# Kernel optimization log

Measured on AMD Instinct MI355X. Metric: run time of the kernel, lower is better.

## Reference

```python
import jax, jax.numpy as jnp
import numpy as np

N = 50000      # nodes
E = 800000     # edges
D_IN = 128
HID = 32
HEADS = 4
D_OUT = 64
NEG_SLOPE = 0.2  # DGL GATConv default


def gat_layer(feat, W, attn_l, attn_r, bias, src, dst, H, F):
    """One DGL-style GATConv layer. feat:[N,in], W:[in,H*F], attn:[H,F], bias:[H*F]."""
    n = feat.shape[0]
    hp = (feat @ W).reshape(n, H, F)                      # projected features [N,H,F]
    el = jnp.sum(hp * attn_l, axis=-1)                    # [N,H]
    er = jnp.sum(hp * attn_r, axis=-1)                    # [N,H]
    e = jax.nn.leaky_relu(el[src] + er[dst], NEG_SLOPE)   # per-edge score [E,H]
    # segment softmax over incoming edges of each dst node
    m = jax.ops.segment_max(e, dst, num_segments=n)       # [N,H]
    a = jnp.exp(e - m[dst])
    denom = jax.ops.segment_sum(a, dst, num_segments=n)   # [N,H]
    alpha = a / denom[dst]                                # [E,H]
    msg = alpha[:, :, None] * hp[src]                     # [E,H,F]
    out = jax.ops.segment_sum(msg, dst, num_segments=n)   # [N,H,F]
    return out + bias.reshape(1, H, F)


def setup_inputs() -> dict:
    key = jax.random.key(0)
    ks = jax.random.split(key, 12)
    s = 0.05
    x = jax.random.normal(ks[0], (N, D_IN), dtype=jnp.float32)
    src = jax.random.randint(ks[1], (E,), 0, N)
    dst = jax.random.randint(ks[2], (E,), 0, N)
    # layer 1: D_IN -> HID with HEADS heads
    W1 = jax.random.normal(ks[3], (D_IN, HEADS * HID), dtype=jnp.float32) * s
    al1 = jax.random.normal(ks[4], (HEADS, HID), dtype=jnp.float32) * s
    ar1 = jax.random.normal(ks[5], (HEADS, HID), dtype=jnp.float32) * s
    b1 = jnp.zeros((HEADS * HID,), dtype=jnp.float32)
    # layer 2: HID*HEADS -> D_OUT with 1 head
    W2 = jax.random.normal(ks[6], (HID * HEADS, D_OUT), dtype=jnp.float32) * s
    al2 = jax.random.normal(ks[7], (1, D_OUT), dtype=jnp.float32) * s
    ar2 = jax.random.normal(ks[8], (1, D_OUT), dtype=jnp.float32) * s
    b2 = jnp.zeros((D_OUT,), dtype=jnp.float32)
    return {"x": x, "W1": W1, "al1": al1, "ar1": ar1, "b1": b1,
            "W2": W2, "al2": al2, "ar2": ar2, "b2": b2,
            "src": src, "dst": dst}


def reference(x, W1, al1, ar1, b1, W2, al2, ar2, b2, src, dst):
    h1 = gat_layer(x, W1, al1, ar1, b1, src, dst, HEADS, HID)   # [N,HEADS,HID]
    h1 = h1.reshape(N, HEADS * HID)                              # concat heads
    h2 = gat_layer(h1, W2, al2, ar2, b2, src, dst, 1, D_OUT)     # [N,1,D_OUT]
    return h2.reshape(N, D_OUT)                                  # squeeze head dim
```

## Files before the change

kernel.cpp:

```cpp
#include <hip/hip_runtime.h>

#define NEG_SLOPE 0.2f

static __device__ __forceinline__ unsigned short f2bf(float f) {
  unsigned x = __float_as_uint(f);
  return (unsigned short)((x + 0x7FFFu + ((x >> 16) & 1u)) >> 16);
}
static __device__ __forceinline__ float bf2f(unsigned short u) {
  return __uint_as_float((unsigned)u << 16);
}

template<int NCOLS, int H>
__global__ __launch_bounds__(256) void gemm_eler(const float* __restrict__ A,
    const float* __restrict__ B, const float* __restrict__ al, const float* __restrict__ ar,
    unsigned short* __restrict__ hb, float* __restrict__ el, float* __restrict__ er, int M) {
  constexpr int K = 128;
  constexpr int TM = 64;
  constexpr int F = NCOLS / H;
  __shared__ float As[TM][K];
  const int tid = threadIdx.x;
  const int m0 = blockIdx.x * TM;

  for (int i = tid; i < TM * K / 4; i += 256) {
    const int m = (i * 4) / K, k = (i * 4) % K;
    float4 v = make_float4(0.f, 0.f, 0.f, 0.f);
    if (m0 + m < M) v = *reinterpret_cast<const float4*>(&A[(size_t)(m0 + m) * K + k]);
    *reinterpret_cast<float4*>(&As[m][k]) = v;
  }
  __syncthreads();

  constexpr int CW = NCOLS / 32;
  const int c0 = (tid & 31) * CW;
  const int n0 = (tid >> 5) * 8;
  float acc[8][CW];
  #pragma unroll
  for (int i = 0; i < 8; ++i)
    #pragma unroll
    for (int j = 0; j < CW; ++j) acc[i][j] = 0.f;

  #pragma unroll 4
  for (int k = 0; k < K; ++k) {
    float wv[CW];
    if constexpr (CW == 4)
      *reinterpret_cast<float4*>(&wv[0]) = *reinterpret_cast<const float4*>(&B[(size_t)k * NCOLS + c0]);
    else
      *reinterpret_cast<float2*>(&wv[0]) = *reinterpret_cast<const float2*>(&B[(size_t)k * NCOLS + c0]);
    float xv[8];
    #pragma unroll
    for (int i = 0; i < 8; ++i) xv[i] = As[n0 + i][k];
    #pragma unroll
    for (int i = 0; i < 8; ++i)
      #pragma unroll
      for (int j = 0; j < CW; ++j)
        acc[i][j] = fmaf(xv[i], wv[j], acc[i][j]);
  }

  float alv[CW], arv[CW];
  if constexpr (CW == 4) {
    *reinterpret_cast<float4*>(&alv[0]) = *reinterpret_cast<const float4*>(&al[c0]);
    *reinterpret_cast<float4*>(&arv[0]) = *reinterpret_cast<const float4*>(&ar[c0]);
  } else {
    *reinterpret_cast<float2*>(&alv[0]) = *reinterpret_cast<const float2*>(&al[c0]);
    *reinterpret_cast<float2*>(&arv[0]) = *reinterpret_cast<const float2*>(&ar[c0]);
  }
  constexpr int GRP = F / CW;
  const int h = c0 / F;

  #pragma unroll
  for (int i = 0; i < 8; ++i) {
    const int m = m0 + n0 + i;
    if (m < M) {
      if constexpr (CW == 4) {
        ushort4 u;
        u.x = f2bf(acc[i][0]); u.y = f2bf(acc[i][1]);
        u.z = f2bf(acc[i][2]); u.w = f2bf(acc[i][3]);
        *reinterpret_cast<ushort4*>(&hb[(size_t)m * NCOLS + c0]) = u;
      } else {
        ushort2 u;
        u.x = f2bf(acc[i][0]); u.y = f2bf(acc[i][1]);
        *reinterpret_cast<ushort2*>(&hb[(size_t)m * NCOLS + c0]) = u;
      }
    }
    float pl = 0.f, pr = 0.f;
    #pragma unroll
    for (int j = 0; j < CW; ++j) {
      pl = fmaf(alv[j], acc[i][j], pl);
      pr = fmaf(arv[j], acc[i][j], pr);
    }
    #pragma unroll
    for (int off = 1; off < GRP; off <<= 1) {
      pl += __shfl_xor(pl, off);
      pr += __shfl_xor(pr, off);
    }
    if (((tid & 31) & (GRP - 1)) == 0 && m < M) {
      el[(size_t)m * H + h] = pl;
      er[(size_t)m * H + h] = pr;
    }
  }
}

__global__ __launch_bounds__(256) void rank_kernel(const int* __restrict__ dst,
    int* deg, int* __restrict__ rank, int E) {
  const int e = blockIdx.x * 256 + threadIdx.x;
  if (e < E) rank[e] = atomicAdd(&deg[dst[e]], 1);
}

__global__ __launch_bounds__(256) void block_sum_kernel(const int* __restrict__ deg,
    int* __restrict__ partials, int N) {
  __shared__ int wsum[4];
  const int tid = threadIdx.x;
  const int base = blockIdx.x * 1024 + tid * 4;
  int s = 0;
  #pragma unroll
  for (int j = 0; j < 4; ++j) if (base + j < N) s += deg[base + j];
  #pragma unroll
  for (int off = 32; off >= 1; off >>= 1) s += __shfl_down(s, off);
  if ((tid & 63) == 0) wsum[tid >> 6] = s;
  __syncthreads();
  if (tid == 0) partials[blockIdx.x] = wsum[0] + wsum[1] + wsum[2] + wsum[3];
}

__global__ __launch_bounds__(64) void scan_partials_kernel(int* partials, int nb) {
  const int tid = threadIdx.x;
  int v = (tid < nb) ? partials[tid] : 0;
  int incl = v;
  #pragma unroll
  for (int off = 1; off < 64; off <<= 1) {
    const int t = __shfl_up(incl, off);
    if (tid >= off) incl += t;
  }
  if (tid < nb) partials[tid] = incl - v;
}

__global__ __launch_bounds__(256) void block_scan_kernel(const int* __restrict__ deg,
    const int* __restrict__ partials, int* __restrict__ row_ptr, int N, int E) {
  __shared__ int wtot[4];
  const int tid = threadIdx.x;
  const int lane = tid & 63, wid = tid >> 6;
  const int idx = blockIdx.x * 1024 + tid * 4;
  int v[4];
  #pragma unroll
  for (int j = 0; j < 4; ++j) v[j] = (idx + j < N) ? deg[idx + j] : 0;
  const int tsum = v[0] + v[1] + v[2] + v[3];
  int incl = tsum;
  #pragma unroll
  for (int off = 1; off < 64; off <<= 1) {
    const int t = __shfl_up(incl, off);
    if (lane >= off) incl += t;
  }
  if (lane == 63) wtot[wid] = incl;
  __syncthreads();
  int excl = partials[blockIdx.x] + incl - tsum;
  for (int w = 0; w < wid; ++w) excl += wtot[w];
  #pragma unroll
  for (int j = 0; j < 4; ++j) {
    if (idx + j < N) { row_ptr[idx + j] = excl; excl += v[j]; }
  }
  if (blockIdx.x == 0 && tid == 0) row_ptr[N] = E;
}

__global__ __launch_bounds__(256) void place_kernel(const int* __restrict__ src,
    const int* __restrict__ dst, const int* __restrict__ row_ptr,
    const int* __restrict__ rank, unsigned short* __restrict__ csr_src, int E) {
  const int e = blockIdx.x * 256 + threadIdx.x;
  if (e < E) {
    csr_src[row_ptr[dst[e]] + rank[e]] = (unsigned short)src[e];
  }
}

template<int H, int F, int NPW>
__global__ __launch_bounds__(256) void gat_agg(const int* __restrict__ row_ptr,
    const unsigned short* __restrict__ csr_src, const float* __restrict__ el,
    const float* __restrict__ er, const unsigned short* __restrict__ hb,
    const float* __restrict__ bias, float* __restrict__ out, int N) {
  constexpr int HF = H * F;
  constexpr int LPN = 64 / NPW;
  constexpr int CPL = HF / LPN;
  static_assert(CPL == 4, "CPL must be 4");
  const int wid = threadIdx.x >> 6;
  const int lane = threadIdx.x & 63;
  const int g = lane / LPN;
  const int gl = lane % LPN;
  const int d = (blockIdx.x * 4 + wid) * NPW + g;
  if (d >= N) return;
  const int c0 = gl * CPL;
  const int h = c0 / F;
  const float erd = er[(size_t)d * H + h];
  const int beg = row_ptr[d], end = row_ptr[d + 1];
  float a0 = 0.f, a1 = 0.f, a2 = 0.f, a3 = 0.f, denom = 0.f;
  int i = beg;

  for (; i + 8 <= end; i += 8) {
    int s[8];
    #pragma unroll
    for (int j = 0; j < 8; ++j) s[j] = csr_src[i + j];
    float ee[8];
    #pragma unroll
    for (int j = 0; j < 8; ++j) ee[j] = el[(size_t)s[j] * H + h];
    ushort4 u[8];
    #pragma unroll
    for (int j = 0; j < 8; ++j)
      u[j] = *reinterpret_cast<const ushort4*>(&hb[(size_t)s[j] * HF + c0]);
    #pragma unroll
    for (int j = 0; j < 8; ++j) {
      float t = ee[j] + erd;
      t = fmaxf(t, NEG_SLOPE * t);
      const float x = __expf(t);
      denom += x;
      a0 = fmaf(x, bf2f(u[j].x), a0); a1 = fmaf(x, bf2f(u[j].y), a1);
      a2 = fmaf(x, bf2f(u[j].z), a2); a3 = fmaf(x, bf2f(u[j].w), a3);
    }
  }
  for (; i + 4 <= end; i += 4) {
    int s[4];
    #pragma unroll
    for (int j = 0; j < 4; ++j) s[j] = csr_src[i + j];
    float ee[4];
    #pragma unroll
    for (int j = 0; j < 4; ++j) ee[j] = el[(size_t)s[j] * H + h];
    ushort4 u[4];
    #pragma unroll
    for (int j = 0; j < 4; ++j)
      u[j] = *reinterpret_cast<const ushort4*>(&hb[(size_t)s[j] * HF + c0]);
    #pragma unroll
    for (int j = 0; j < 4; ++j) {
      float t = ee[j] + erd;
      t = fmaxf(t, NEG_SLOPE * t);
      const float x = __expf(t);
      denom += x;
      a0 = fmaf(x, bf2f(u[j].x), a0); a1 = fmaf(x, bf2f(u[j].y), a1);
      a2 = fmaf(x, bf2f(u[j].z), a2); a3 = fmaf(x, bf2f(u[j].w), a3);
    }
  }
  for (; i < end; ++i) {
    const int s = csr_src[i];
    float t = el[(size_t)s * H + h] + erd;
    t = fmaxf(t, NEG_SLOPE * t);
    const float x = __expf(t);
    denom += x;
    const ushort4 u = *reinterpret_cast<const ushort4*>(&hb[(size_t)s * HF + c0]);
    a0 = fmaf(x, bf2f(u.x), a0); a1 = fmaf(x, bf2f(u.y), a1);
    a2 = fmaf(x, bf2f(u.z), a2); a3 = fmaf(x, bf2f(u.w), a3);
  }

  const float inv = denom > 0.f ? 1.f / denom : 0.f;
  const float4 bv = *reinterpret_cast<const float4*>(&bias[c0]);
  float4 o;
  o.x = bv.x + a0 * inv; o.y = bv.y + a1 * inv;
  o.z = bv.z + a2 * inv; o.w = bv.w + a3 * inv;
  *reinterpret_cast<float4*>(&out[(size_t)d * HF + c0]) = o;
}

extern "C" void kernel_launch(void* const* d_in, const int* in_sizes, int n_in,
                              void* d_out, int out_size, void* d_ws, size_t ws_size,
                              hipStream_t stream) {
  const float* x   = (const float*)d_in[0];
  const float* W1  = (const float*)d_in[1];
  const float* al1 = (const float*)d_in[2];
  const float* ar1 = (const float*)d_in[3];
  const float* b1  = (const float*)d_in[4];
  const float* W2  = (const float*)d_in[5];
  const float* al2 = (const float*)d_in[6];
  const float* ar2 = (const float*)d_in[7];
  const float* b2  = (const float*)d_in[8];
  const int* src   = (const int*)d_in[9];
  const int* dst   = (const int*)d_in[10];
  const int N = in_sizes[0] / 128;
  const int E = in_sizes[9];
  float* out = (float*)d_out;

  float* ws   = (float*)d_ws;
  float* out1 = ws;
  float* el1  = out1 + (size_t)N * 128;
  float* er1  = el1 + (size_t)N * 4;
  float* el2  = er1 + (size_t)N * 4;
  float* er2  = el2 + N;
  int* deg     = (int*)(er2 + N);
  int* row_ptr = deg + N;
  int* rank    = row_ptr + N + 1;
  unsigned short* csr_src = (unsigned short*)(rank + E);
  int* partials = (int*)(csr_src + ((E + 1) & ~1));
  unsigned short* hb1 = (unsigned short*)(partials + 64);
  unsigned short* hb2 = hb1 + (size_t)N * 128;

  const dim3 blk(256);
  const int nb = (N + 1023) / 1024;

  hipMemsetAsync(deg, 0, (size_t)N * sizeof(int), stream);
  rank_kernel<<<dim3((E + 255) / 256), blk, 0, stream>>>(dst, deg, rank, E);
  block_sum_kernel<<<dim3(nb), blk, 0, stream>>>(deg, partials, N);
  scan_partials_kernel<<<dim3(1), dim3(64), 0, stream>>>(partials, nb);
  block_scan_kernel<<<dim3(nb), blk, 0, stream>>>(deg, partials, row_ptr, N, E);
  place_kernel<<<dim3((E + 255) / 256), blk, 0, stream>>>(src, dst, row_ptr, rank, csr_src, E);

  gemm_eler<128, 4><<<dim3((N + 63) / 64), blk, 0, stream>>>(x, W1, al1, ar1, hb1, el1, er1, N);
  gat_agg<4, 32, 2><<<dim3((N + 7) / 8), blk, 0, stream>>>(row_ptr, csr_src, el1, er1, hb1, b1, out1, N);

  gemm_eler<64, 1><<<dim3((N + 63) / 64), blk, 0, stream>>>(out1, W2, al2, ar2, hb2, el2, er2, N);
  gat_agg<1, 64, 4><<<dim3((N + 15) / 16), blk, 0, stream>>>(row_ptr, csr_src, el2, er2, hb2, b2, out, N);
}
```

Before: 186.1 us.

## Fuse degree-rank atomics into layer-1 GEMM launch and unroll aggregation by 16

Merges the edge rank/degree-count kernel into the first projection GEMM launch by adding extra blocks that take the rank path, so the two independent workloads overlap in one grid and one launch disappears. The layer-2 GEMM reuses the same kernel with zero rank blocks. The aggregation kernel gains a 16-edge unrolled loop ahead of the 8-edge loop, raising memory-level parallelism at the cost of more registers and possibly lower occupancy.

```diff
diff --git a/kernel.cpp b/kernel.cpp
--- a/kernel.cpp
+++ b/kernel.cpp
@@ -11,16 +11,23 @@
 }
 
 template<int NCOLS, int H>
-__global__ __launch_bounds__(256) void gemm_eler(const float* __restrict__ A,
+__global__ __launch_bounds__(256) void gemm_eler_rank(const float* __restrict__ A,
     const float* __restrict__ B, const float* __restrict__ al, const float* __restrict__ ar,
-    unsigned short* __restrict__ hb, float* __restrict__ el, float* __restrict__ er, int M) {
+    unsigned short* __restrict__ hb, float* __restrict__ el, float* __restrict__ er, int M,
+    int gemmBlocks, const int* __restrict__ dst, int* deg, int* __restrict__ rank, int E) {
   constexpr int K = 128;
   constexpr int TM = 64;
   constexpr int F = NCOLS / H;
   __shared__ float As[TM][K];
   const int tid = threadIdx.x;
+
+  if (blockIdx.x >= gemmBlocks) {
+    const int e = (blockIdx.x - gemmBlocks) * 256 + tid;
+    if (e < E) rank[e] = atomicAdd(&deg[dst[e]], 1);
+    return;
+  }
+
   const int m0 = blockIdx.x * TM;
-
   for (int i = tid; i < TM * K / 4; i += 256) {
     const int m = (i * 4) / K, k = (i * 4) % K;
     float4 v = make_float4(0.f, 0.f, 0.f, 0.f);
@@ -97,12 +104,6 @@
       er[(size_t)m * H + h] = pr;
     }
   }
-}
-
-__global__ __launch_bounds__(256) void rank_kernel(const int* __restrict__ dst,
-    int* deg, int* __restrict__ rank, int E) {
-  const int e = blockIdx.x * 256 + threadIdx.x;
-  if (e < E) rank[e] = atomicAdd(&deg[dst[e]], 1);
 }
 
 __global__ __launch_bounds__(256) void block_sum_kernel(const int* __restrict__ deg,
@@ -190,6 +191,27 @@
   float a0 = 0.f, a1 = 0.f, a2 = 0.f, a3 = 0.f, denom = 0.f;
   int i = beg;
 
+  for (; i + 16 <= end; i += 16) {
+    int s[16];
+    #pragma unroll
+    for (int j = 0; j < 16; ++j) s[j] = csr_src[i + j];
+    float ee[16];
+    #pragma unroll
+    for (int j = 0; j < 16; ++j) ee[j] = el[(size_t)s[j] * H + h];
+    ushort4 u[16];
+    #pragma unroll
+    for (int j = 0; j < 16; ++j)
+      u[j] = *reinterpret_cast<const ushort4*>(&hb[(size_t)s[j] * HF + c0]);
+    #pragma unroll
+    for (int j = 0; j < 16; ++j) {
+      float t = ee[j] + erd;
+      t = fmaxf(t, NEG_SLOPE * t);
+      const float x = __expf(t);
+      denom += x;
+      a0 = fmaf(x, bf2f(u[j].x), a0); a1 = fmaf(x, bf2f(u[j].y), a1);
+      a2 = fmaf(x, bf2f(u[j].z), a2); a3 = fmaf(x, bf2f(u[j].w), a3);
+    }
+  }
   for (; i + 8 <= end; i += 8) {
     int s[8];
     #pragma unroll
@@ -285,17 +307,21 @@
 
   const dim3 blk(256);
   const int nb = (N + 1023) / 1024;
+  const int gemmBlocks = (N + 63) / 64;
+  const int rankBlocks = (E + 255) / 256;
 
   hipMemsetAsync(deg, 0, (size_t)N * sizeof(int), stream);
-  rank_kernel<<<dim3((E + 255) / 256), blk, 0, stream>>>(dst, deg, rank, E);
+  gemm_eler_rank<128, 4><<<dim3(gemmBlocks + rankBlocks), blk, 0, stream>>>(
+      x, W1, al1, ar1, hb1, el1, er1, N, gemmBlocks, dst, deg, rank, E);
+
   block_sum_kernel<<<dim3(nb), blk, 0, stream>>>(deg, partials, N);
   scan_partials_kernel<<<dim3(1), dim3(64), 0, stream>>>(partials, nb);
   block_scan_kernel<<<dim3(nb), blk, 0, stream>>>(deg, partials, row_ptr, N, E);
-  place_kernel<<<dim3((E + 255) / 256), blk, 0, stream>>>(src, dst, row_ptr, rank, csr_src, E);
-
-  gemm_eler<128, 4><<<dim3((N + 63) / 64), blk, 0, stream>>>(x, W1, al1, ar1, hb1, el1, er1, N);
+  place_kernel<<<dim3(rankBlocks), blk, 0, stream>>>(src, dst, row_ptr, rank, csr_src, E);
+
   gat_agg<4, 32, 2><<<dim3((N + 7) / 8), blk, 0, stream>>>(row_ptr, csr_src, el1, er1, hb1, b1, out1, N);
 
-  gemm_eler<64, 1><<<dim3((N + 63) / 64), blk, 0, stream>>>(out1, W2, al2, ar2, hb2, el2, er2, N);
+  gemm_eler_rank<64, 1><<<dim3(gemmBlocks), blk, 0, stream>>>(
+      out1, W2, al2, ar2, hb2, el2, er2, N, gemmBlocks, dst, deg, rank, 0);
   gat_agg<1, 64, 4><<<dim3((N + 15) / 16), blk, 0, stream>>>(row_ptr, csr_src, el2, er2, hb2, b2, out, N);
 }
```

Result: faster. 168.6 us (-9.4%).
